# Optimization experiments

Measured on AMD Instinct MI355X. Metric: run time of the kernel, lower is better.

The kernel has to match this reference:

```python
import jax, jax.numpy as jnp
import numpy as np

LATENT = 128
N_NODES = 50000
N_EDGES = 800000
LN_EPS = 1e-5


def _glorot(key, fan_in, fan_out):
    lim = np.sqrt(6.0 / (fan_in + fan_out)).astype(np.float32)
    return jax.random.uniform(key, (fan_in, fan_out), jnp.float32, -lim, lim)


def setup_inputs() -> dict:
    key = jax.random.key(0)
    ks = jax.random.split(key, 10)
    node_latents = jax.random.normal(ks[0], (1, N_NODES, LATENT), jnp.float32)
    mesh_edge_latents = jax.random.normal(ks[1], (1, N_EDGES, LATENT), jnp.float32)
    senders = jax.random.randint(ks[2], (N_EDGES,), 0, N_NODES, jnp.int32)
    receivers = jax.random.randint(ks[3], (N_EDGES,), 0, N_NODES, jnp.int32)
    # mesh_edge_net: Linear(3L, L), ReLU, Linear(L, L), ReLU, LayerNorm(L)
    me_w1 = _glorot(ks[4], 3 * LATENT, LATENT)
    me_b1 = jnp.zeros((LATENT,), jnp.float32)
    me_w2 = _glorot(ks[5], LATENT, LATENT)
    me_b2 = jnp.zeros((LATENT,), jnp.float32)
    me_g = jnp.ones((LATENT,), jnp.float32)
    me_beta = jnp.zeros((LATENT,), jnp.float32)
    # node_feature_net: Linear(2L, L), ReLU, Linear(L, L), ReLU, LayerNorm(L)
    nf_w1 = _glorot(ks[6], 2 * LATENT, LATENT)
    nf_b1 = jnp.zeros((LATENT,), jnp.float32)
    nf_w2 = _glorot(ks[7], LATENT, LATENT)
    nf_b2 = jnp.zeros((LATENT,), jnp.float32)
    nf_g = jnp.ones((LATENT,), jnp.float32)
    nf_beta = jnp.zeros((LATENT,), jnp.float32)
    return dict(node_latents=node_latents, mesh_edge_latents=mesh_edge_latents,
                senders=senders, receivers=receivers,
                me_w1=me_w1, me_b1=me_b1, me_w2=me_w2, me_b2=me_b2, me_g=me_g, me_beta=me_beta,
                nf_w1=nf_w1, nf_b1=nf_b1, nf_w2=nf_w2, nf_b2=nf_b2, nf_g=nf_g, nf_beta=nf_beta)


def _mlp_ln(x, w1, b1, w2, b2, g, beta):
    h = jax.nn.relu(x @ w1 + b1)
    h = jax.nn.relu(h @ w2 + b2)
    mu = jnp.mean(h, axis=-1, keepdims=True)
    var = jnp.var(h, axis=-1, keepdims=True)
    return (h - mu) * jax.lax.rsqrt(var + LN_EPS) * g + beta


def reference(node_latents, mesh_edge_latents, senders, receivers,
              me_w1, me_b1, me_w2, me_b2, me_g, me_beta,
              nf_w1, nf_b1, nf_w2, nf_b2, nf_g, nf_beta):
    # gather sender/receiver node features: [B, E, L]
    edge_in = jnp.concatenate([node_latents[:, senders, :],
                               node_latents[:, receivers, :],
                               mesh_edge_latents], axis=-1)
    new_edges = _mlp_ln(edge_in, me_w1, me_b1, me_w2, me_b2, me_g, me_beta)
    # scatter_add messages to receiver nodes along dim=1
    aggr = jax.vmap(lambda e: jax.ops.segment_sum(e, receivers, num_segments=N_NODES))(new_edges)
    node_in = jnp.concatenate([node_latents, aggr], axis=-1)
    new_nodes = _mlp_ln(node_in, nf_w1, nf_b1, nf_w2, nf_b2, nf_g, nf_beta)
    new_nodes = new_nodes + node_latents  # residual
    new_edges = new_edges + mesh_edge_latents  # residual
    return new_nodes, new_edges
```

## Files before the change

kernel.cpp:

```cpp
#include <hip/hip_runtime.h>
#include <stdint.h>

typedef unsigned short u16;
typedef __bf16 bf16x8 __attribute__((ext_vector_type(8)));
typedef float f32x4 __attribute__((ext_vector_type(4)));

#define N_NODES 50000
#define N_EDGES 800000
#define LN_EPS 1e-5f

__device__ __forceinline__ float bf2f(u16 u) {
    union { unsigned int i; float f; } c; c.i = ((unsigned int)u) << 16; return c.f;
}
__device__ __forceinline__ u16 f2bf(float f) {
    union { float f; unsigned int i; } c; c.f = f;
    unsigned int r = c.i + 0x7FFFu + ((c.i >> 16) & 1u);
    return (u16)(r >> 16);
}
__device__ __forceinline__ uint4 pack8(const float* __restrict__ p) {
    const float4 f0 = ((const float4*)p)[0];
    const float4 f1 = ((const float4*)p)[1];
    union { u16 u[8]; uint4 q; } t;
    t.u[0] = f2bf(f0.x); t.u[1] = f2bf(f0.y); t.u[2] = f2bf(f0.z); t.u[3] = f2bf(f0.w);
    t.u[4] = f2bf(f1.x); t.u[5] = f2bf(f1.y); t.u[6] = f2bf(f1.z); t.u[7] = f2bf(f1.w);
    return t.q;
}

template<int KB>
__device__ __forceinline__ void load_wfrag(const float* __restrict__ W, int n_base, int lane,
                                           bf16x8 (&wf)[KB][2]) {
    const int kq = (lane >> 4) * 8;
    const int cl = lane & 15;
#pragma unroll
    for (int kb = 0; kb < KB; ++kb) {
#pragma unroll
        for (int n = 0; n < 2; ++n) {
            const float* p = W + (size_t)(kb * 32 + kq) * 128 + (n_base + n * 16 + cl);
            union { u16 u[8]; bf16x8 v; } t;
#pragma unroll
            for (int j = 0; j < 8; ++j) t.u[j] = f2bf(p[j * 128]);
            wf[kb][n] = t.v;
        }
    }
}

__global__ __launch_bounds__(256, 2)
void edge_mlp_kernel(const float* __restrict__ node, const float* __restrict__ elat,
                     const int* __restrict__ senders, const int* __restrict__ receivers,
                     const float* __restrict__ w1, const float* __restrict__ b1,
                     const float* __restrict__ w2, const float* __restrict__ b2,
                     const float* __restrict__ gam, const float* __restrict__ bet,
                     float* __restrict__ eout, float* __restrict__ aggr)
{
    __shared__ __align__(16) u16 x_lds[3 * 64 * 128];
    __shared__ __align__(16) u16 h_lds[64 * 128];

    float2* part = (float2*)x_lds;
    float* muv = (float*)(x_lds + 1024);
    float* rsv = (float*)(x_lds + 1152);

    const int tid = threadIdx.x;
    const int w = tid >> 6;
    const int lane = tid & 63;
    const int cl = lane & 15;
    const int q = lane >> 4;
    const int n_base = w * 32;

    bf16x8 w1f[12][2], w2f[4][2];
    load_wfrag<12>(w1, n_base, lane, w1f);
    load_wfrag<4>(w2, n_base, lane, w2f);
    float b1v[2], b2v[2], gv[2], bv[2];
#pragma unroll
    for (int n = 0; n < 2; ++n) {
        const int c = n_base + n * 16 + cl;
        b1v[n] = b1[c]; b2v[n] = b2[c];
        gv[n]  = gam[c]; bv[n] = bet[c];
    }

    for (int tile = blockIdx.x; tile < N_EDGES / 64; tile += gridDim.x) {
        const int base = tile * 64;

        {
            const int ch = tid & 15;
            const int r0 = tid >> 4;
#pragma unroll
            for (int gp = 0; gp < 4; ++gp) {
                const int row = gp * 16 + r0;
                const int rx = row & 7;
                const int sn = senders[base + row];
                const int rc = receivers[base + row];
                uint4* dst = (uint4*)x_lds + row * 16;
                dst[(ch ^ rx)]        = pack8(node + (size_t)sn * 128 + ch * 8);
                dst[1024 + (ch ^ rx)] = pack8(node + (size_t)rc * 128 + ch * 8);
                dst[2048 + (ch ^ rx)] = pack8(elat + (size_t)(base + row) * 128 + ch * 8);
            }
        }
        __syncthreads();

        f32x4 acc[4][2];
#pragma unroll
        for (int m = 0; m < 4; ++m)
#pragma unroll
            for (int n = 0; n < 2; ++n)
#pragma unroll
                for (int r = 0; r < 4; ++r) acc[m][n][r] = 0.f;

#pragma unroll
        for (int kb = 0; kb < 12; ++kb) {
            const int p = kb >> 2, k2 = kb & 3;
            bf16x8 a[4];
#pragma unroll
            for (int m = 0; m < 4; ++m) {
                const int row = m * 16 + cl;
                a[m] = __builtin_bit_cast(bf16x8,
                    ((const uint4*)x_lds)[p * 1024 + row * 16 + ((k2 * 4 + q) ^ (row & 7))]);
            }
#pragma unroll
            for (int m = 0; m < 4; ++m)
#pragma unroll
                for (int n = 0; n < 2; ++n)
                    acc[m][n] = __builtin_amdgcn_mfma_f32_16x16x32_bf16(a[m], w1f[kb][n], acc[m][n], 0, 0, 0);
        }

#pragma unroll
        for (int m = 0; m < 4; ++m)
#pragma unroll
            for (int n = 0; n < 2; ++n)
#pragma unroll
                for (int r = 0; r < 4; ++r) {
                    const int row = m * 16 + q * 4 + r;
                    const int col = n_base + n * 16 + cl;
                    const float v = fmaxf(acc[m][n][r] + b1v[n], 0.f);
                    h_lds[row * 128 + (((col >> 3) ^ (row & 7)) << 3) + (col & 7)] = f2bf(v);
                }
        __syncthreads();

#pragma unroll
        for (int m = 0; m < 4; ++m)
#pragma unroll
            for (int n = 0; n < 2; ++n)
#pragma unroll
                for (int r = 0; r < 4; ++r) acc[m][n][r] = 0.f;
#pragma unroll
        for (int kb = 0; kb < 4; ++kb) {
            bf16x8 a[4];
#pragma unroll
            for (int m = 0; m < 4; ++m) {
                const int row = m * 16 + cl;
                a[m] = __builtin_bit_cast(bf16x8,
                    ((const uint4*)h_lds)[row * 16 + ((kb * 4 + q) ^ (row & 7))]);
            }
#pragma unroll
            for (int m = 0; m < 4; ++m)
#pragma unroll
                for (int n = 0; n < 2; ++n)
                    acc[m][n] = __builtin_amdgcn_mfma_f32_16x16x32_bf16(a[m], w2f[kb][n], acc[m][n], 0, 0, 0);
        }

#pragma unroll
        for (int m = 0; m < 4; ++m)
#pragma unroll
            for (int n = 0; n < 2; ++n)
#pragma unroll
                for (int r = 0; r < 4; ++r)
                    acc[m][n][r] = fmaxf(acc[m][n][r] + b2v[n], 0.f);

#pragma unroll
        for (int m = 0; m < 4; ++m)
#pragma unroll
            for (int r = 0; r < 4; ++r) {
                float s  = acc[m][0][r] + acc[m][1][r];
                float ss = acc[m][0][r] * acc[m][0][r] + acc[m][1][r] * acc[m][1][r];
#pragma unroll
                for (int off = 1; off < 16; off <<= 1) {
                    s  += __shfl_xor(s, off, 64);
                    ss += __shfl_xor(ss, off, 64);
                }
                if (cl == 0) part[w * 64 + m * 16 + q * 4 + r] = make_float2(s, ss);
            }
        __syncthreads();
        if (tid < 64) {
            float s = 0.f, ss = 0.f;
#pragma unroll
            for (int ww = 0; ww < 4; ++ww) { const float2 pp = part[ww * 64 + tid]; s += pp.x; ss += pp.y; }
            const float mu = s * (1.f / 128.f);
            const float var = ss * (1.f / 128.f) - mu * mu;
            muv[tid] = mu;
            rsv[tid] = rsqrtf(var + LN_EPS);
        }
        __syncthreads();

#pragma unroll
        for (int m = 0; m < 4; ++m)
#pragma unroll
            for (int r = 0; r < 4; ++r) {
                const int row = m * 16 + q * 4 + r;
                const float mu = muv[row];
                const float rs = rsv[row];
                const int rc = receivers[base + row];
                float* orow = eout + (size_t)(base + row) * 128;
#pragma unroll
                for (int n = 0; n < 2; ++n) {
                    const int col = n_base + n * 16 + cl;
                    const float ln = (acc[m][n][r] - mu) * rs * gv[n] + bv[n];
                    atomicAdd(&aggr[(size_t)rc * 128 + col], ln);
                    const float e = bf2f(x_lds[16384 + row * 128 + (((col >> 3) ^ (row & 7)) << 3) + (col & 7)]);
                    orow[col] = ln + e;
                }
            }
        __syncthreads();
    }
}

__global__ __launch_bounds__(256, 2)
void node_mlp_kernel(const float* __restrict__ node, const float* __restrict__ aggr,
                     const float* __restrict__ w1, const float* __restrict__ b1,
                     const float* __restrict__ w2, const float* __restrict__ b2,
                     const float* __restrict__ gam, const float* __restrict__ bet,
                     float* __restrict__ nout)
{
    __shared__ __align__(16) u16 x_lds[2 * 64 * 128];
    __shared__ __align__(16) u16 h_lds[64 * 128];
    __shared__ float2 part[256];
    __shared__ float muv[64], rsv[64];

    const int tid = threadIdx.x;
    const int w = tid >> 6;
    const int lane = tid & 63;
    const int cl = lane & 15;
    const int q = lane >> 4;
    const int n_base = w * 32;

    bf16x8 w1f[8][2], w2f[4][2];
    load_wfrag<8>(w1, n_base, lane, w1f);
    load_wfrag<4>(w2, n_base, lane, w2f);
    float b1v[2], b2v[2], gv[2], bv[2];
#pragma unroll
    for (int n = 0; n < 2; ++n) {
        const int c = n_base + n * 16 + cl;
        b1v[n] = b1[c]; b2v[n] = b2[c];
        gv[n]  = gam[c]; bv[n] = bet[c];
    }

    const int ntiles = (N_NODES + 63) / 64;
    for (int tile = blockIdx.x; tile < ntiles; tile += gridDim.x) {
        const int base = tile * 64;

        {
            const int ch = tid & 15;
            const int r0 = tid >> 4;
#pragma unroll
            for (int gp = 0; gp < 4; ++gp) {
                const int row = gp * 16 + r0;
                const int rx = row & 7;
                int gn = base + row;
                if (gn >= N_NODES) gn = N_NODES - 1;
                uint4* dst = (uint4*)x_lds + row * 16;
                dst[(ch ^ rx)]        = pack8(node + (size_t)gn * 128 + ch * 8);
                dst[1024 + (ch ^ rx)] = pack8(aggr + (size_t)gn * 128 + ch * 8);
            }
        }
        __syncthreads();

        f32x4 acc[4][2];
#pragma unroll
        for (int m = 0; m < 4; ++m)
#pragma unroll
            for (int n = 0; n < 2; ++n)
#pragma unroll
                for (int r = 0; r < 4; ++r) acc[m][n][r] = 0.f;
#pragma unroll
        for (int kb = 0; kb < 8; ++kb) {
            const int p = kb >> 2, k2 = kb & 3;
            bf16x8 a[4];
#pragma unroll
            for (int m = 0; m < 4; ++m) {
                const int row = m * 16 + cl;
                a[m] = __builtin_bit_cast(bf16x8,
                    ((const uint4*)x_lds)[p * 1024 + row * 16 + ((k2 * 4 + q) ^ (row & 7))]);
            }
#pragma unroll
            for (int m = 0; m < 4; ++m)
#pragma unroll
                for (int n = 0; n < 2; ++n)
                    acc[m][n] = __builtin_amdgcn_mfma_f32_16x16x32_bf16(a[m], w1f[kb][n], acc[m][n], 0, 0, 0);
        }
#pragma unroll
        for (int m = 0; m < 4; ++m)
#pragma unroll
            for (int n = 0; n < 2; ++n)
#pragma unroll
                for (int r = 0; r < 4; ++r) {
                    const int row = m * 16 + q * 4 + r;
                    const int col = n_base + n * 16 + cl;
                    const float v = fmaxf(acc[m][n][r] + b1v[n], 0.f);
                    h_lds[row * 128 + (((col >> 3) ^ (row & 7)) << 3) + (col & 7)] = f2bf(v);
                }
        __syncthreads();

#pragma unroll
        for (int m = 0; m < 4; ++m)
#pragma unroll
            for (int n = 0; n < 2; ++n)
#pragma unroll
                for (int r = 0; r < 4; ++r) acc[m][n][r] = 0.f;
#pragma unroll
        for (int kb = 0; kb < 4; ++kb) {
            bf16x8 a[4];
#pragma unroll
            for (int m = 0; m < 4; ++m) {
                const int row = m * 16 + cl;
                a[m] = __builtin_bit_cast(bf16x8,
                    ((const uint4*)h_lds)[row * 16 + ((kb * 4 + q) ^ (row & 7))]);
            }
#pragma unroll
            for (int m = 0; m < 4; ++m)
#pragma unroll
                for (int n = 0; n < 2; ++n)
                    acc[m][n] = __builtin_amdgcn_mfma_f32_16x16x32_bf16(a[m], w2f[kb][n], acc[m][n], 0, 0, 0);
        }
#pragma unroll
        for (int m = 0; m < 4; ++m)
#pragma unroll
            for (int n = 0; n < 2; ++n)
#pragma unroll
                for (int r = 0; r < 4; ++r)
                    acc[m][n][r] = fmaxf(acc[m][n][r] + b2v[n], 0.f);

#pragma unroll
        for (int m = 0; m < 4; ++m)
#pragma unroll
            for (int r = 0; r < 4; ++r) {
                float s  = acc[m][0][r] + acc[m][1][r];
                float ss = acc[m][0][r] * acc[m][0][r] + acc[m][1][r] * acc[m][1][r];
#pragma unroll
                for (int off = 1; off < 16; off <<= 1) {
                    s  += __shfl_xor(s, off, 64);
                    ss += __shfl_xor(ss, off, 64);
                }
                if (cl == 0) part[w * 64 + m * 16 + q * 4 + r] = make_float2(s, ss);
            }
        __syncthreads();
        if (tid < 64) {
            float s = 0.f, ss = 0.f;
#pragma unroll
            for (int ww = 0; ww < 4; ++ww) { const float2 pp = part[ww * 64 + tid]; s += pp.x; ss += pp.y; }
            const float mu = s * (1.f / 128.f);
            const float var = ss * (1.f / 128.f) - mu * mu;
            muv[tid] = mu;
            rsv[tid] = rsqrtf(var + LN_EPS);
        }
        __syncthreads();

#pragma unroll
        for (int m = 0; m < 4; ++m)
#pragma unroll
            for (int r = 0; r < 4; ++r) {
                const int row = m * 16 + q * 4 + r;
                if (base + row < N_NODES) {
                    const float mu = muv[row];
                    const float rs = rsv[row];
                    float* orow = nout + (size_t)(base + row) * 128;
#pragma unroll
                    for (int n = 0; n < 2; ++n) {
                        const int col = n_base + n * 16 + cl;
                        const float ln = (acc[m][n][r] - mu) * rs * gv[n] + bv[n];
                        const float e = bf2f(x_lds[row * 128 + (((col >> 3) ^ (row & 7)) << 3) + (col & 7)]);
                        orow[col] = ln + e;
                    }
                }
            }
        __syncthreads();
    }
}

extern "C" void kernel_launch(void* const* d_in, const int* in_sizes, int n_in,
                              void* d_out, int out_size, void* d_ws, size_t ws_size,
                              hipStream_t stream) {
    (void)in_sizes; (void)n_in; (void)out_size;
    const float* node = (const float*)d_in[0];
    const float* elat = (const float*)d_in[1];
    const int* senders = (const int*)d_in[2];
    const int* receivers = (const int*)d_in[3];
    const float* me_w1 = (const float*)d_in[4];
    const float* me_b1 = (const float*)d_in[5];
    const float* me_w2 = (const float*)d_in[6];
    const float* me_b2 = (const float*)d_in[7];
    const float* me_g  = (const float*)d_in[8];
    const float* me_be = (const float*)d_in[9];
    const float* nf_w1 = (const float*)d_in[10];
    const float* nf_b1 = (const float*)d_in[11];
    const float* nf_w2 = (const float*)d_in[12];
    const float* nf_b2 = (const float*)d_in[13];
    const float* nf_g  = (const float*)d_in[14];
    const float* nf_be = (const float*)d_in[15];

    float* out_nodes = (float*)d_out;
    float* out_edges = out_nodes + (size_t)N_NODES * 128;
    float* aggr = (float*)d_ws;
    const size_t aggr_bytes = (size_t)N_NODES * 128 * sizeof(float);
    if (ws_size < aggr_bytes) return;

    hipMemsetAsync(aggr, 0, aggr_bytes, stream);
    edge_mlp_kernel<<<512, 256, 0, stream>>>(node, elat, senders, receivers,
                                             me_w1, me_b1, me_w2, me_b2, me_g, me_be,
                                             out_edges, aggr);
    node_mlp_kernel<<<782, 256, 0, stream>>>(node, aggr,
                                             nf_w1, nf_b1, nf_w2, nf_b2, nf_g, nf_be,
                                             out_nodes);
}
```

Measured before the change: 938.6 us.

## Stream pre-packed bf16 weights from global instead of holding them in registers

Adds a small kernel that converts and packs the four weight matrices into MFMA fragment layout once per call. The edge and node MLP kernels now stream weight fragments from global/L2 with a two-step prefetch instead of keeping all fragments resident in registers. They also reuse the input LDS buffer for the hidden activations and cache receiver indices in LDS. This frees registers and LDS so occupancy can rise (launch bounds 3 and 4, edge grid 768), at the cost of reloading weights from cache on every tile and an extra kernel launch.

```diff
diff --git a/kernel.cpp b/kernel.cpp
--- a/kernel.cpp
+++ b/kernel.cpp
@@ -9,55 +9,50 @@
 #define N_EDGES 800000
 #define LN_EPS 1e-5f
 
-__device__ __forceinline__ float bf2f(u16 u) {
-    union { unsigned int i; float f; } c; c.i = ((unsigned int)u) << 16; return c.f;
-}
-__device__ __forceinline__ u16 f2bf(float f) {
-    union { float f; unsigned int i; } c; c.f = f;
-    unsigned int r = c.i + 0x7FFFu + ((c.i >> 16) & 1u);
-    return (u16)(r >> 16);
-}
 __device__ __forceinline__ uint4 pack8(const float* __restrict__ p) {
     const float4 f0 = ((const float4*)p)[0];
     const float4 f1 = ((const float4*)p)[1];
-    union { u16 u[8]; uint4 q; } t;
-    t.u[0] = f2bf(f0.x); t.u[1] = f2bf(f0.y); t.u[2] = f2bf(f0.z); t.u[3] = f2bf(f0.w);
-    t.u[4] = f2bf(f1.x); t.u[5] = f2bf(f1.y); t.u[6] = f2bf(f1.z); t.u[7] = f2bf(f1.w);
+    union { __bf16 b[8]; uint4 q; } t;
+    t.b[0] = (__bf16)f0.x; t.b[1] = (__bf16)f0.y; t.b[2] = (__bf16)f0.z; t.b[3] = (__bf16)f0.w;
+    t.b[4] = (__bf16)f1.x; t.b[5] = (__bf16)f1.y; t.b[6] = (__bf16)f1.z; t.b[7] = (__bf16)f1.w;
     return t.q;
 }
 
-template<int KB>
-__device__ __forceinline__ void load_wfrag(const float* __restrict__ W, int n_base, int lane,
-                                           bf16x8 (&wf)[KB][2]) {
-    const int kq = (lane >> 4) * 8;
-    const int cl = lane & 15;
-#pragma unroll
-    for (int kb = 0; kb < KB; ++kb) {
-#pragma unroll
-        for (int n = 0; n < 2; ++n) {
-            const float* p = W + (size_t)(kb * 32 + kq) * 128 + (n_base + n * 16 + cl);
-            union { u16 u[8]; bf16x8 v; } t;
-#pragma unroll
-            for (int j = 0; j < 8; ++j) t.u[j] = f2bf(p[j * 128]);
-            wf[kb][n] = t.v;
-        }
-    }
+__global__ void pack_weights(const float* __restrict__ w1e, const float* __restrict__ w2e,
+                             const float* __restrict__ w1n, const float* __restrict__ w2n,
+                             uint4* __restrict__ out)
+{
+    const int t = blockIdx.x * 256 + threadIdx.x;
+    const float* W; int idx;
+    if (t < 6144)       { W = w1e; idx = t; }
+    else if (t < 8192)  { W = w2e; idx = t - 6144; }
+    else if (t < 12288) { W = w1n; idx = t - 8192; }
+    else                { W = w2n; idx = t - 12288; }
+    const int lane = idx & 63;
+    const int col16 = (idx >> 6) & 7;
+    const int kb = idx >> 9;
+    const int row0 = kb * 32 + (lane >> 4) * 8;
+    const int col = col16 * 16 + (lane & 15);
+    union { __bf16 b[8]; uint4 q; } v;
+#pragma unroll
+    for (int j = 0; j < 8; ++j) v.b[j] = (__bf16)W[(size_t)(row0 + j) * 128 + col];
+    out[t] = v.q;
 }
 
-__global__ __launch_bounds__(256, 2)
+__global__ __launch_bounds__(256, 3)
 void edge_mlp_kernel(const float* __restrict__ node, const float* __restrict__ elat,
                      const int* __restrict__ senders, const int* __restrict__ receivers,
-                     const float* __restrict__ w1, const float* __restrict__ b1,
-                     const float* __restrict__ w2, const float* __restrict__ b2,
+                     const float* __restrict__ b1, const float* __restrict__ b2,
                      const float* __restrict__ gam, const float* __restrict__ bet,
+                     const uint4* __restrict__ w1p, const uint4* __restrict__ w2p,
                      float* __restrict__ eout, float* __restrict__ aggr)
 {
     __shared__ __align__(16) u16 x_lds[3 * 64 * 128];
-    __shared__ __align__(16) u16 h_lds[64 * 128];
-
-    float2* part = (float2*)x_lds;
-    float* muv = (float*)(x_lds + 1024);
-    float* rsv = (float*)(x_lds + 1152);
+    __shared__ int rcv_s[64];
+
+    float2* part = (float2*)(x_lds + 8192);
+    float*  muv  = (float*)(x_lds + 8192 + 1024);
+    float*  rsv  = (float*)(x_lds + 8192 + 1152);
 
     const int tid = threadIdx.x;
     const int w = tid >> 6;
@@ -66,9 +61,6 @@
     const int q = lane >> 4;
     const int n_base = w * 32;
 
-    bf16x8 w1f[12][2], w2f[4][2];
-    load_wfrag<12>(w1, n_base, lane, w1f);
-    load_wfrag<4>(w2, n_base, lane, w2f);
     float b1v[2], b2v[2], gv[2], bv[2];
 #pragma unroll
     for (int n = 0; n < 2; ++n) {
@@ -89,8 +81,9 @@
                 const int rx = row & 7;
                 const int sn = senders[base + row];
                 const int rc = receivers[base + row];
+                if (ch == 0) rcv_s[row] = rc;
                 uint4* dst = (uint4*)x_lds + row * 16;
-                dst[(ch ^ rx)]        = pack8(node + (size_t)sn * 128 + ch * 8);
+                dst[ch ^ rx]          = pack8(node + (size_t)sn * 128 + ch * 8);
                 dst[1024 + (ch ^ rx)] = pack8(node + (size_t)rc * 128 + ch * 8);
                 dst[2048 + (ch ^ rx)] = pack8(elat + (size_t)(base + row) * 128 + ch * 8);
             }
@@ -105,8 +98,20 @@
 #pragma unroll
                 for (int r = 0; r < 4; ++r) acc[m][n][r] = 0.f;
 
+        uint4 wreg[14][2];
+#pragma unroll
+        for (int kb = 0; kb < 2; ++kb)
+#pragma unroll
+            for (int n = 0; n < 2; ++n)
+                wreg[kb][n] = w1p[(kb * 8 + w * 2 + n) * 64 + lane];
+
 #pragma unroll
         for (int kb = 0; kb < 12; ++kb) {
+            if (kb + 2 < 12) {
+#pragma unroll
+                for (int n = 0; n < 2; ++n)
+                    wreg[kb + 2][n] = w1p[((kb + 2) * 8 + w * 2 + n) * 64 + lane];
+            }
             const int p = kb >> 2, k2 = kb & 3;
             bf16x8 a[4];
 #pragma unroll
@@ -119,20 +124,33 @@
             for (int m = 0; m < 4; ++m)
 #pragma unroll
                 for (int n = 0; n < 2; ++n)
-                    acc[m][n] = __builtin_amdgcn_mfma_f32_16x16x32_bf16(a[m], w1f[kb][n], acc[m][n], 0, 0, 0);
-        }
-
-#pragma unroll
-        for (int m = 0; m < 4; ++m)
-#pragma unroll
-            for (int n = 0; n < 2; ++n)
-#pragma unroll
-                for (int r = 0; r < 4; ++r) {
-                    const int row = m * 16 + q * 4 + r;
-                    const int col = n_base + n * 16 + cl;
-                    const float v = fmaxf(acc[m][n][r] + b1v[n], 0.f);
-                    h_lds[row * 128 + (((col >> 3) ^ (row & 7)) << 3) + (col & 7)] = f2bf(v);
-                }
+                    acc[m][n] = __builtin_amdgcn_mfma_f32_16x16x32_bf16(
+                        a[m], __builtin_bit_cast(bf16x8, wreg[kb][n]), acc[m][n], 0, 0, 0);
+        }
+
+        uint4 w2reg[4][2];
+#pragma unroll
+        for (int kb = 0; kb < 4; ++kb)
+#pragma unroll
+            for (int n = 0; n < 2; ++n)
+                w2reg[kb][n] = w2p[(kb * 8 + w * 2 + n) * 64 + lane];
+
+        __syncthreads();
+
+        {
+            __bf16* hb = (__bf16*)x_lds;
+#pragma unroll
+            for (int m = 0; m < 4; ++m)
+#pragma unroll
+                for (int n = 0; n < 2; ++n)
+#pragma unroll
+                    for (int r = 0; r < 4; ++r) {
+                        const int row = m * 16 + q * 4 + r;
+                        const int col = n_base + n * 16 + cl;
+                        hb[row * 128 + (((col >> 3) ^ (row & 7)) << 3) + (col & 7)] =
+                            (__bf16)fmaxf(acc[m][n][r] + b1v[n], 0.f);
+                    }
+        }
         __syncthreads();
 
 #pragma unroll
@@ -148,13 +166,14 @@
             for (int m = 0; m < 4; ++m) {
                 const int row = m * 16 + cl;
                 a[m] = __builtin_bit_cast(bf16x8,
-                    ((const uint4*)h_lds)[row * 16 + ((kb * 4 + q) ^ (row & 7))]);
-            }
-#pragma unroll
-            for (int m = 0; m < 4; ++m)
-#pragma unroll
-                for (int n = 0; n < 2; ++n)
-                    acc[m][n] = __builtin_amdgcn_mfma_f32_16x16x32_bf16(a[m], w2f[kb][n], acc[m][n], 0, 0, 0);
+                    ((const uint4*)x_lds)[row * 16 + ((kb * 4 + q) ^ (row & 7))]);
+            }
+#pragma unroll
+            for (int m = 0; m < 4; ++m)
+#pragma unroll
+                for (int n = 0; n < 2; ++n)
+                    acc[m][n] = __builtin_amdgcn_mfma_f32_16x16x32_bf16(
+                        a[m], __builtin_bit_cast(bf16x8, w2reg[kb][n]), acc[m][n], 0, 0, 0);
         }
 
 #pragma unroll
@@ -197,14 +216,14 @@
                 const int row = m * 16 + q * 4 + r;
                 const float mu = muv[row];
                 const float rs = rsv[row];
-                const int rc = receivers[base + row];
+                const int rc = rcv_s[row];
                 float* orow = eout + (size_t)(base + row) * 128;
 #pragma unroll
                 for (int n = 0; n < 2; ++n) {
                     const int col = n_base + n * 16 + cl;
                     const float ln = (acc[m][n][r] - mu) * rs * gv[n] + bv[n];
                     atomicAdd(&aggr[(size_t)rc * 128 + col], ln);
-                    const float e = bf2f(x_lds[16384 + row * 128 + (((col >> 3) ^ (row & 7)) << 3) + (col & 7)]);
+                    const float e = (float)((__bf16*)x_lds)[16384 + row * 128 + (((col >> 3) ^ (row & 7)) << 3) + (col & 7)];
                     orow[col] = ln + e;
                 }
             }
@@ -212,15 +231,14 @@
     }
 }
 
-__global__ __launch_bounds__(256, 2)
+__global__ __launch_bounds__(256, 4)
 void node_mlp_kernel(const float* __restrict__ node, const float* __restrict__ aggr,
-                     const float* __restrict__ w1, const float* __restrict__ b1,
-                     const float* __restrict__ w2, const float* __restrict__ b2,
+                     const float* __restrict__ b1, const float* __restrict__ b2,
                      const float* __restrict__ gam, const float* __restrict__ bet,
+                     const uint4* __restrict__ w1p, const uint4* __restrict__ w2p,
                      float* __restrict__ nout)
 {
     __shared__ __align__(16) u16 x_lds[2 * 64 * 128];
-    __shared__ __align__(16) u16 h_lds[64 * 128];
     __shared__ float2 part[256];
     __shared__ float muv[64], rsv[64];
 
@@ -231,9 +249,6 @@
     const int q = lane >> 4;
     const int n_base = w * 32;
 
-    bf16x8 w1f[8][2], w2f[4][2];
-    load_wfrag<8>(w1, n_base, lane, w1f);
-    load_wfrag<4>(w2, n_base, lane, w2f);
     float b1v[2], b2v[2], gv[2], bv[2];
 #pragma unroll
     for (int n = 0; n < 2; ++n) {
@@ -256,7 +271,7 @@
                 int gn = base + row;
                 if (gn >= N_NODES) gn = N_NODES - 1;
                 uint4* dst = (uint4*)x_lds + row * 16;
-                dst[(ch ^ rx)]        = pack8(node + (size_t)gn * 128 + ch * 8);
+                dst[ch ^ rx]          = pack8(node + (size_t)gn * 128 + ch * 8);
                 dst[1024 + (ch ^ rx)] = pack8(aggr + (size_t)gn * 128 + ch * 8);
             }
         }
@@ -269,8 +284,21 @@
             for (int n = 0; n < 2; ++n)
 #pragma unroll
                 for (int r = 0; r < 4; ++r) acc[m][n][r] = 0.f;
+
+        uint4 wreg[10][2];
+#pragma unroll
+        for (int kb = 0; kb < 2; ++kb)
+#pragma unroll
+            for (int n = 0; n < 2; ++n)
+                wreg[kb][n] = w1p[(kb * 8 + w * 2 + n) * 64 + lane];
+
 #pragma unroll
         for (int kb = 0; kb < 8; ++kb) {
+            if (kb + 2 < 8) {
+#pragma unroll
+                for (int n = 0; n < 2; ++n)
+                    wreg[kb + 2][n] = w1p[((kb + 2) * 8 + w * 2 + n) * 64 + lane];
+            }
             const int p = kb >> 2, k2 = kb & 3;
             bf16x8 a[4];
 #pragma unroll
@@ -283,19 +311,33 @@
             for (int m = 0; m < 4; ++m)
 #pragma unroll
                 for (int n = 0; n < 2; ++n)
-                    acc[m][n] = __builtin_amdgcn_mfma_f32_16x16x32_bf16(a[m], w1f[kb][n], acc[m][n], 0, 0, 0);
-        }
-#pragma unroll
-        for (int m = 0; m < 4; ++m)
-#pragma unroll
-            for (int n = 0; n < 2; ++n)
-#pragma unroll
-                for (int r = 0; r < 4; ++r) {
-                    const int row = m * 16 + q * 4 + r;
-                    const int col = n_base + n * 16 + cl;
-                    const float v = fmaxf(acc[m][n][r] + b1v[n], 0.f);
-                    h_lds[row * 128 + (((col >> 3) ^ (row & 7)) << 3) + (col & 7)] = f2bf(v);
-                }
+                    acc[m][n] = __builtin_amdgcn_mfma_f32_16x16x32_bf16(
+                        a[m], __builtin_bit_cast(bf16x8, wreg[kb][n]), acc[m][n], 0, 0, 0);
+        }
+
+        uint4 w2reg[4][2];
+#pragma unroll
+        for (int kb = 0; kb < 4; ++kb)
+#pragma unroll
+            for (int n = 0; n < 2; ++n)
+                w2reg[kb][n] = w2p[(kb * 8 + w * 2 + n) * 64 + lane];
+
+        __syncthreads();
+
+        {
+            __bf16* hb = (__bf16*)(x_lds + 8192);
+#pragma unroll
+            for (int m = 0; m < 4; ++m)
+#pragma unroll
+                for (int n = 0; n < 2; ++n)
+#pragma unroll
+                    for (int r = 0; r < 4; ++r) {
+                        const int row = m * 16 + q * 4 + r;
+                        const int col = n_base + n * 16 + cl;
+                        hb[row * 128 + (((col >> 3) ^ (row & 7)) << 3) + (col & 7)] =
+                            (__bf16)fmaxf(acc[m][n][r] + b1v[n], 0.f);
+                    }
+        }
         __syncthreads();
 
 #pragma unroll
@@ -311,13 +353,14 @@
             for (int m = 0; m < 4; ++m) {
                 const int row = m * 16 + cl;
                 a[m] = __builtin_bit_cast(bf16x8,
-                    ((const uint4*)h_lds)[row * 16 + ((kb * 4 + q) ^ (row & 7))]);
-            }
-#pragma unroll
-            for (int m = 0; m < 4; ++m)
-#pragma unroll
-                for (int n = 0; n < 2; ++n)
-                    acc[m][n] = __builtin_amdgcn_mfma_f32_16x16x32_bf16(a[m], w2f[kb][n], acc[m][n], 0, 0, 0);
+                    ((const uint4*)x_lds)[1024 + row * 16 + ((kb * 4 + q) ^ (row & 7))]);
+            }
+#pragma unroll
+            for (int m = 0; m < 4; ++m)
+#pragma unroll
+                for (int n = 0; n < 2; ++n)
+                    acc[m][n] = __builtin_amdgcn_mfma_f32_16x16x32_bf16(
+                        a[m], __builtin_bit_cast(bf16x8, w2reg[kb][n]), acc[m][n], 0, 0, 0);
         }
 #pragma unroll
         for (int m = 0; m < 4; ++m)
@@ -365,7 +408,7 @@
                     for (int n = 0; n < 2; ++n) {
                         const int col = n_base + n * 16 + cl;
                         const float ln = (acc[m][n][r] - mu) * rs * gv[n] + bv[n];
-                        const float e = bf2f(x_lds[row * 128 + (((col >> 3) ^ (row & 7)) << 3) + (col & 7)]);
+                        const float e = (float)((__bf16*)x_lds)[row * 128 + (((col >> 3) ^ (row & 7)) << 3) + (col & 7)];
                         orow[col] = ln + e;
                     }
                 }
@@ -399,13 +442,17 @@
     float* out_edges = out_nodes + (size_t)N_NODES * 128;
     float* aggr = (float*)d_ws;
     const size_t aggr_bytes = (size_t)N_NODES * 128 * sizeof(float);
-    if (ws_size < aggr_bytes) return;
+    uint4* wpack = (uint4*)((char*)d_ws + aggr_bytes);
+    if (ws_size < aggr_bytes + 14336 * sizeof(uint4)) return;
 
     hipMemsetAsync(aggr, 0, aggr_bytes, stream);
-    edge_mlp_kernel<<<512, 256, 0, stream>>>(node, elat, senders, receivers,
-                                             me_w1, me_b1, me_w2, me_b2, me_g, me_be,
+    pack_weights<<<56, 256, 0, stream>>>(me_w1, me_w2, nf_w1, nf_w2, wpack);
+    edge_mlp_kernel<<<768, 256, 0, stream>>>(node, elat, senders, receivers,
+                                             me_b1, me_b2, me_g, me_be,
+                                             wpack, wpack + 6144,
                                              out_edges, aggr);
     node_mlp_kernel<<<782, 256, 0, stream>>>(node, aggr,
-                                             nf_w1, nf_b1, nf_w2, nf_b2, nf_g, nf_be,
+                                             nf_b1, nf_b2, nf_g, nf_be,
+                                             wpack + 8192, wpack + 12288,
                                              out_nodes);
 }
```

New measurement: 1.009 ms. +7.4%, slower.
